# Performance work log

Measured on AMD Instinct MI355X. Metric: run time of the kernel, lower is better.

Reference implementation:

```python
import jax, jax.numpy as jnp
import numpy as np

NUM_LAYER = 5
EMB = 256
N = 100000
E = 300000
SELF_LOOP_BOND = 4
BN_EPS = 1e-5


def setup_inputs() -> dict:
    key = jax.random.key(0)
    ks = jax.random.split(key, 16)
    f = lambda k, shape: jax.random.normal(k, shape, jnp.float32) * 0.02
    return {
        "x_atom": jax.random.randint(ks[0], (N,), 0, 120),
        "x_chir": jax.random.randint(ks[1], (N,), 0, 3),
        "edge_index": jax.random.randint(ks[2], (2, E), 0, N),
        "edge_bond": jax.random.randint(ks[3], (E,), 0, 4),
        "edge_dir": jax.random.randint(ks[4], (E,), 0, 3),
        "atom_emb": f(ks[5], (120, EMB)),
        "chir_emb": f(ks[6], (3, EMB)),
        "bond_embs": f(ks[7], (NUM_LAYER, 6, EMB)),
        "dir_embs": f(ks[8], (NUM_LAYER, 3, EMB)),
        "W1s": f(ks[9], (NUM_LAYER, 2 * EMB, EMB)),
        "b1s": f(ks[10], (NUM_LAYER, 2 * EMB)),
        "W2s": f(ks[11], (NUM_LAYER, EMB, 2 * EMB)),
        "b2s": f(ks[12], (NUM_LAYER, EMB)),
        "bn_w": jnp.ones((NUM_LAYER, EMB), jnp.float32),
        "bn_b": jnp.zeros((NUM_LAYER, EMB), jnp.float32),
    }


def reference(x_atom, x_chir, edge_index, edge_bond, edge_dir,
              atom_emb, chir_emb, bond_embs, dir_embs,
              W1s, b1s, W2s, b2s, bn_w, bn_b):
    n = x_atom.shape[0]
    src, dst = edge_index[0], edge_index[1]
    # add self loops (edge_attr = [4, 0] for each node)
    loop = jnp.arange(n)
    src_full = jnp.concatenate([src, loop])          # [E+N]
    dst_full = jnp.concatenate([dst, loop])          # [E+N]
    bond_full = jnp.concatenate([edge_bond, jnp.full((n,), SELF_LOOP_BOND, edge_bond.dtype)])
    dir_full = jnp.concatenate([edge_dir, jnp.zeros((n,), edge_dir.dtype)])

    # initial node features: atom + chirality embeddings
    h = atom_emb[x_atom] + chir_emb[x_chir]          # [N, EMB]

    for l in range(NUM_LAYER):
        # per-layer edge embeddings (bond type + bond direction)
        e_emb = bond_embs[l][bond_full] + dir_embs[l][dir_full]   # [E+N, EMB]
        # message = x_j + edge_attr; aggregate = scatter-add to dst
        msg = h[src_full] + e_emb                                  # gather
        agg = jax.ops.segment_sum(msg, dst_full, num_segments=n)  # scatter-add
        # update MLP: Linear(EMB->2EMB) -> ReLU -> Linear(2EMB->EMB)
        hmid = jax.nn.relu(agg @ W1s[l].T + b1s[l])                # [N, 2EMB]
        h2 = hmid @ W2s[l].T + b2s[l]                              # [N, EMB]
        # batch norm (training mode: batch statistics, biased variance)
        mean = h2.mean(axis=0)
        var = h2.var(axis=0)
        h2 = (h2 - mean) * jax.lax.rsqrt(var + BN_EPS) * bn_w[l] + bn_b[l]
        # relu on all but last layer; dropout with p=0 is identity
        if l < NUM_LAYER - 1:
            h2 = jax.nn.relu(h2)
        h = h2
    # JK == 'last'
    return h
```

## Files before the change

kernel.cpp:

```cpp
#include <hip/hip_runtime.h>

#define EMB 256
#define NLAYER 5
#define CHUNK 1024

typedef unsigned int u32;
typedef unsigned short u16;

typedef __bf16 bf16x8 __attribute__((ext_vector_type(8)));
typedef float f32x4 __attribute__((ext_vector_type(4)));

__device__ __forceinline__ float bf2f(u16 u) {
    union { u32 i; float f; } x; x.i = ((u32)u) << 16; return x.f;
}
__device__ __forceinline__ u16 f2bf(float f) {
    union { float f; u32 i; } x; x.f = f;
    u32 r = x.i + 0x7FFFu + ((x.i >> 16) & 1u);
    return (u16)(r >> 16);
}
__device__ __forceinline__ void unpack4(uint2 p, float* o) {
    union { u32 i; float f; } a, b, c, d;
    a.i = p.x << 16; b.i = p.x & 0xFFFF0000u;
    c.i = p.y << 16; d.i = p.y & 0xFFFF0000u;
    o[0] = a.f; o[1] = b.f; o[2] = c.f; o[3] = d.f;
}

__global__ void k_detect(const u32* __restrict__ bnw_raw, int* __restrict__ flag) {
    if (threadIdx.x == 0 && blockIdx.x == 0)
        *flag = (bnw_raw[0] == 0x3F803F80u) ? 1 : 0;
}

struct Cvt { const void* s; u16* d; int n; };
struct CvtTab { Cvt t[10]; };

__global__ void k_convert(CvtTab tab, const int* __restrict__ flag, int maxn) {
    int f = *flag;
    int stride = gridDim.x * blockDim.x;
    for (int i = blockIdx.x * blockDim.x + threadIdx.x; i < maxn; i += stride) {
        for (int j = 0; j < 10; j++) {
            if (i < tab.t[j].n) {
                u16 v;
                if (f) v = ((const u16*)tab.t[j].s)[i];
                else   v = f2bf(((const float*)tab.t[j].s)[i]);
                tab.t[j].d[i] = v;
            }
        }
    }
}

__global__ void k_zero(u32* p, int n) {
    int i = blockIdx.x * blockDim.x + threadIdx.x;
    if (i < n) p[i] = 0u;
}

__global__ void k_hist(const int* __restrict__ eidx, const int* __restrict__ ebond,
                       const int* __restrict__ edir,
                       u32* __restrict__ cnt, u32* __restrict__ cntb, u32* __restrict__ cntd, int E) {
    int e = blockIdx.x * blockDim.x + threadIdx.x;
    if (e >= E) return;
    int dst = eidx[E + e];
    atomicAdd(&cnt[dst], 1u);
    atomicAdd(&cntb[dst * 4 + ebond[e]], 1u);
    atomicAdd(&cntd[dst * 3 + edir[e]], 1u);
}

__global__ void k_chunksum(const u32* __restrict__ cnt, u32* __restrict__ partial, int N) {
    int b = blockIdx.x, t = threadIdx.x;
    int base = b * CHUNK + t * 4;
    u32 s = 0;
    for (int i = 0; i < 4; i++) { int idx = base + i; if (idx < N) s += cnt[idx]; }
    __shared__ u32 red[256];
    red[t] = s; __syncthreads();
    for (int o = 128; o > 0; o >>= 1) { if (t < o) red[t] += red[t + o]; __syncthreads(); }
    if (t == 0) partial[b] = red[0];
}

__global__ void k_scanpartial(u32* partial, u32* indptr, int nch, int N) {
    if (threadIdx.x == 0 && blockIdx.x == 0) {
        u32 run = 0;
        for (int i = 0; i < nch; i++) { u32 x = partial[i]; partial[i] = run; run += x; }
        indptr[N] = run;
    }
}

__global__ void k_chunkscan(const u32* __restrict__ cnt, const u32* __restrict__ partial,
                            u32* __restrict__ indptr, u32* __restrict__ fillp, int N) {
    int b = blockIdx.x, t = threadIdx.x;
    int base = b * CHUNK + t * 4;
    u32 c[4]; u32 tsum = 0;
    for (int i = 0; i < 4; i++) { int idx = base + i; c[i] = (idx < N) ? cnt[idx] : 0u; tsum += c[i]; }
    __shared__ u32 sc[256];
    sc[t] = tsum; __syncthreads();
    for (int o = 1; o < 256; o <<= 1) {
        u32 x = (t >= o) ? sc[t - o] : 0u;
        __syncthreads();
        sc[t] += x;
        __syncthreads();
    }
    u32 run = partial[b] + sc[t] - tsum;
    for (int i = 0; i < 4; i++) {
        int idx = base + i;
        if (idx < N) { indptr[idx] = run; fillp[idx] = run; }
        run += c[i];
    }
}

__global__ void k_fill(const int* __restrict__ eidx, u32* __restrict__ fillp,
                       u32* __restrict__ srcs, int E) {
    int e = blockIdx.x * blockDim.x + threadIdx.x;
    if (e >= E) return;
    int dst = eidx[E + e];
    u32 pos = atomicAdd(&fillp[dst], 1u);
    srcs[pos] = (u32)eidx[e];
}

__global__ void k_h0(const int* __restrict__ xa, const int* __restrict__ xc,
                     const u16* __restrict__ aemb, const u16* __restrict__ cemb,
                     u16* __restrict__ H, int N) {
    int wave = threadIdx.x >> 6, lane = threadIdx.x & 63;
    int v = blockIdx.x * 4 + wave;
    if (v >= N) return;
    int a = xa[v], c = xc[v];
    int c4 = lane * 4;
    uint2 pa = *(const uint2*)(aemb + (size_t)a * EMB + c4);
    uint2 pc = *(const uint2*)(cemb + (size_t)c * EMB + c4);
    float fa[4], fc[4];
    unpack4(pa, fa); unpack4(pc, fc);
    ushort4 ov;
    ov.x = f2bf(fa[0] + fc[0]); ov.y = f2bf(fa[1] + fc[1]);
    ov.z = f2bf(fa[2] + fc[2]); ov.w = f2bf(fa[3] + fc[3]);
    *(ushort4*)(H + (size_t)v * EMB + c4) = ov;
}

__global__ void k_scatter(const u16* __restrict__ H, const u32* __restrict__ indptr,
                          const u32* __restrict__ srcs,
                          const u32* __restrict__ cntb, const u32* __restrict__ cntd,
                          const u16* __restrict__ bemb, const u16* __restrict__ demb,
                          const float* __restrict__ scsh, int relu,
                          u16* __restrict__ AGG, int N) {
    int wave = threadIdx.x >> 6, lane = threadIdx.x & 63;
    int v = blockIdx.x * 4 + wave;
    if (v >= N) return;
    int c4 = lane * 4;
    float sc[4] = {1.f, 1.f, 1.f, 1.f}, sh[4] = {0.f, 0.f, 0.f, 0.f};
    if (scsh) {
        float4 s0 = *(const float4*)(scsh + c4);
        float4 s1 = *(const float4*)(scsh + 256 + c4);
        sc[0] = s0.x; sc[1] = s0.y; sc[2] = s0.z; sc[3] = s0.w;
        sh[0] = s1.x; sh[1] = s1.y; sh[2] = s1.z; sh[3] = s1.w;
    }
    float acc[4] = {0.f, 0.f, 0.f, 0.f};
    u32 beg = indptr[v], end = indptr[v + 1];
    for (u32 e = beg; e < end; e++) {
        u32 s = srcs[e];
        uint2 p = *(const uint2*)(H + (size_t)s * EMB + c4);
        float f[4]; unpack4(p, f);
        for (int i = 0; i < 4; i++) {
            float y = f[i] * sc[i] + sh[i];
            if (relu) y = fmaxf(y, 0.f);
            acc[i] += y;
        }
    }
    {
        uint2 p = *(const uint2*)(H + (size_t)v * EMB + c4);
        float f[4]; unpack4(p, f);
        for (int i = 0; i < 4; i++) {
            float y = f[i] * sc[i] + sh[i];
            if (relu) y = fmaxf(y, 0.f);
            acc[i] += y;
        }
    }
    float cb[5];
    cb[0] = (float)cntb[v * 4 + 0]; cb[1] = (float)cntb[v * 4 + 1];
    cb[2] = (float)cntb[v * 4 + 2]; cb[3] = (float)cntb[v * 4 + 3]; cb[4] = 1.f;
    float cd[3];
    cd[0] = (float)cntd[v * 3 + 0] + 1.f; cd[1] = (float)cntd[v * 3 + 1]; cd[2] = (float)cntd[v * 3 + 2];
    for (int b = 0; b < 5; b++) {
        uint2 p = *(const uint2*)(bemb + b * EMB + c4);
        float f[4]; unpack4(p, f);
        for (int i = 0; i < 4; i++) acc[i] += cb[b] * f[i];
    }
    for (int d = 0; d < 3; d++) {
        uint2 p = *(const uint2*)(demb + d * EMB + c4);
        float f[4]; unpack4(p, f);
        for (int i = 0; i < 4; i++) acc[i] += cd[d] * f[i];
    }
    ushort4 ov;
    ov.x = f2bf(acc[0]); ov.y = f2bf(acc[1]); ov.z = f2bf(acc[2]); ov.w = f2bf(acc[3]);
    *(ushort4*)(AGG + (size_t)v * EMB + c4) = ov;
}

#define KP1 264
#define KB1 40

__global__ __launch_bounds__(256) void k_gemm1(
    const u16* __restrict__ A, const u16* __restrict__ W1, const u16* __restrict__ bias,
    u16* __restrict__ HM, int M) {
    __shared__ __align__(16) u16 As[128 * KP1];
    __shared__ __align__(16) u16 Bs[128 * KB1];
    int m0 = blockIdx.x * 128;
    int t = threadIdx.x;
    int wave = t >> 6, lane = t & 63;
    int wm = (wave >> 1) * 64, wn = (wave & 1) * 64;
    int lr = lane & 15, quad = lane >> 4;

    for (int it = 0; it < 16; it++) {
        int ci = t + it * 256;
        int r = ci >> 5, kc = (ci & 31) * 8;
        int gr = m0 + r; if (gr > M - 1) gr = M - 1;
        *(uint4*)(As + r * KP1 + kc) = *(const uint4*)(A + (size_t)gr * 256 + kc);
    }
    __syncthreads();

    for (int nc = 0; nc < 4; nc++) {
        int n0 = nc * 128;
        f32x4 acc[4][4];
        for (int i = 0; i < 4; i++)
            for (int j = 0; j < 4; j++)
                acc[i][j] = (f32x4){0.f, 0.f, 0.f, 0.f};
        for (int ks = 0; ks < 256; ks += 32) {
            __syncthreads();
            for (int it = 0; it < 2; it++) {
                int ci = t + it * 256;
                int r = ci >> 2, kc = (ci & 3) * 8;
                *(uint4*)(Bs + r * KB1 + kc) = *(const uint4*)(W1 + (size_t)(n0 + r) * 256 + ks + kc);
            }
            __syncthreads();
            bf16x8 af[4], bfr[4];
            for (int i = 0; i < 4; i++)
                af[i] = *(const bf16x8*)(As + (wm + i * 16 + lr) * KP1 + ks + quad * 8);
            for (int j = 0; j < 4; j++)
                bfr[j] = *(const bf16x8*)(Bs + (wn + j * 16 + lr) * KB1 + quad * 8);
            for (int i = 0; i < 4; i++)
                for (int j = 0; j < 4; j++)
                    acc[i][j] = __builtin_amdgcn_mfma_f32_16x16x32_bf16(af[i], bfr[j], acc[i][j], 0, 0, 0);
        }
        for (int j = 0; j < 4; j++) {
            int gn = n0 + wn + j * 16 + lr;
            float bv = bf2f(bias[gn]);
            for (int i = 0; i < 4; i++) {
                int mbase = m0 + wm + i * 16 + quad * 4;
                for (int r = 0; r < 4; r++) {
                    int gm = mbase + r;
                    if (gm < M) {
                        float v = fmaxf(acc[i][j][r] + bv, 0.f);
                        HM[(size_t)gm * 512 + gn] = f2bf(v);
                    }
                }
            }
        }
    }
}

#define LSTR 80

__global__ __launch_bounds__(256) void k_gemm2(
    const u16* __restrict__ A, const u16* __restrict__ B, const u16* __restrict__ bias,
    u16* __restrict__ C, float* __restrict__ S, int M) {
    __shared__ __align__(16) u16 As[128 * LSTR];
    __shared__ __align__(16) u16 Bs[128 * LSTR];
    int n0 = blockIdx.x * 128;
    int m0 = blockIdx.y * 128;
    int t = threadIdx.x;
    int wave = t >> 6, lane = t & 63;
    int wm = (wave >> 1) * 64, wn = (wave & 1) * 64;
    int lr = lane & 15, quad = lane >> 4;

    f32x4 acc[4][4];
    for (int i = 0; i < 4; i++)
        for (int j = 0; j < 4; j++)
            acc[i][j] = (f32x4){0.f, 0.f, 0.f, 0.f};

    for (int k0 = 0; k0 < 512; k0 += 64) {
        for (int it = 0; it < 4; it++) {
            int ci = t + it * 256;
            int r = ci >> 3, kc = (ci & 7) * 8;
            int gr = m0 + r; if (gr > M - 1) gr = M - 1;
            *(uint4*)(As + r * LSTR + kc) = *(const uint4*)(A + (size_t)gr * 512 + k0 + kc);
            *(uint4*)(Bs + r * LSTR + kc) = *(const uint4*)(B + (size_t)(n0 + r) * 512 + k0 + kc);
        }
        __syncthreads();
        for (int ks = 0; ks < 64; ks += 32) {
            bf16x8 af[4], bfr[4];
            for (int i = 0; i < 4; i++)
                af[i] = *(const bf16x8*)(As + (wm + i * 16 + lr) * LSTR + ks + quad * 8);
            for (int j = 0; j < 4; j++)
                bfr[j] = *(const bf16x8*)(Bs + (wn + j * 16 + lr) * LSTR + ks + quad * 8);
            for (int i = 0; i < 4; i++)
                for (int j = 0; j < 4; j++)
                    acc[i][j] = __builtin_amdgcn_mfma_f32_16x16x32_bf16(af[i], bfr[j], acc[i][j], 0, 0, 0);
        }
        __syncthreads();
    }
    for (int j = 0; j < 4; j++) {
        int gn = n0 + wn + j * 16 + lr;
        float bv = bf2f(bias[gn]);
        float s = 0.f, q = 0.f;
        for (int i = 0; i < 4; i++) {
            int mbase = m0 + wm + i * 16 + quad * 4;
            for (int r = 0; r < 4; r++) {
                int gm = mbase + r;
                if (gm < M) {
                    float v = acc[i][j][r] + bv;
                    C[(size_t)gm * 256 + gn] = f2bf(v);
                    s += v; q += v * v;
                }
            }
        }
        s += __shfl_xor(s, 16, 64); s += __shfl_xor(s, 32, 64);
        q += __shfl_xor(q, 16, 64); q += __shfl_xor(q, 32, 64);
        if (quad == 0) {
            atomicAdd(&S[gn], s);
            atomicAdd(&S[256 + gn], q);
        }
    }
}

__global__ void k_finalize(const float* __restrict__ S, const u16* __restrict__ bnw,
                           const u16* __restrict__ bnb, float* __restrict__ scsh, float invN) {
    int c = threadIdx.x;
    float mean = S[c] * invN;
    float var = S[256 + c] * invN - mean * mean;
    var = fmaxf(var, 0.f);
    float inv = rsqrtf(var + 1e-5f);
    float sc = bf2f(bnw[c]) * inv;
    scsh[c] = sc;
    scsh[256 + c] = bf2f(bnb[c]) - mean * sc;
}

__global__ void k_out(const u16* __restrict__ H2, const float* __restrict__ scsh,
                      void* __restrict__ out, const int* __restrict__ flag, int N) {
    int wave = threadIdx.x >> 6, lane = threadIdx.x & 63;
    int v = blockIdx.x * 4 + wave;
    if (v >= N) return;
    int c4 = lane * 4;
    float4 s0 = *(const float4*)(scsh + c4);
    float4 s1 = *(const float4*)(scsh + 256 + c4);
    uint2 p = *(const uint2*)(H2 + (size_t)v * EMB + c4);
    float f[4]; unpack4(p, f);
    float o0 = f[0] * s0.x + s1.x;
    float o1 = f[1] * s0.y + s1.y;
    float o2 = f[2] * s0.z + s1.z;
    float o3 = f[3] * s0.w + s1.w;
    if (*flag) {
        ushort4 ov;
        ov.x = f2bf(o0); ov.y = f2bf(o1); ov.z = f2bf(o2); ov.w = f2bf(o3);
        *(ushort4*)((u16*)out + (size_t)v * EMB + c4) = ov;
    } else {
        float4 ov = make_float4(o0, o1, o2, o3);
        *(float4*)((float*)out + (size_t)v * EMB + c4) = ov;
    }
}

extern "C" void kernel_launch(void* const* d_in, const int* in_sizes, int n_in,
                              void* d_out, int out_size, void* d_ws, size_t ws_size,
                              hipStream_t stream) {
    const int* x_atom = (const int*)d_in[0];
    const int* x_chir = (const int*)d_in[1];
    const int* eidx   = (const int*)d_in[2];
    const int* ebond  = (const int*)d_in[3];
    const int* edir   = (const int*)d_in[4];

    const int N = in_sizes[0];
    const int E = in_sizes[3];

    char* p = (char*)d_ws;
    size_t off = 0;
    auto alloc = [&](size_t bytes) -> void* {
        void* r = p + off;
        off += bytes;
        off = (off + 255) & ~(size_t)255;
        return r;
    };
    u16* X   = (u16*)alloc((size_t)N * EMB * 2);
    u16* Y   = (u16*)alloc((size_t)N * EMB * 2);
    u16* HM  = (u16*)alloc((size_t)N * 512 * 2);
    u32* cz  = (u32*)alloc(((size_t)8 * N + NLAYER * 512) * 4);
    u32* cnt  = cz;
    u32* cntb = cz + N;
    u32* cntd = cz + 5 * (size_t)N;
    float* stats5 = (float*)(cz + 8 * (size_t)N);
    u32* indptr = (u32*)alloc((size_t)(N + 1) * 4);
    u32* fillp  = (u32*)alloc((size_t)N * 4);
    u32* srcs   = (u32*)alloc((size_t)E * 4);
    u32* partial = (u32*)alloc(256 * 4);
    float* scsh  = (float*)alloc(512 * 4);
    int* flag    = (int*)alloc(256);

    int csz[10] = {120 * EMB, 3 * EMB, NLAYER * 6 * EMB, NLAYER * 3 * EMB,
                   NLAYER * 512 * EMB, NLAYER * 512, NLAYER * EMB * 512, NLAYER * EMB,
                   NLAYER * EMB, NLAYER * EMB};
    u16* cbuf[10];
    for (int j = 0; j < 10; j++) cbuf[j] = (u16*)alloc((size_t)csz[j] * 2);
    u16* atom_emb  = cbuf[0];
    u16* chir_emb  = cbuf[1];
    u16* bond_embs = cbuf[2];
    u16* dir_embs  = cbuf[3];
    u16* W1s = cbuf[4];
    u16* b1s = cbuf[5];
    u16* W2s = cbuf[6];
    u16* b2s = cbuf[7];
    u16* bnw = cbuf[8];
    u16* bnb = cbuf[9];

    const int nodeBlocks = (N + 3) / 4;
    const int nch = (N + CHUNK - 1) / CHUNK;

    k_detect<<<1, 64, 0, stream>>>((const u32*)d_in[13], flag);
    {
        CvtTab tab;
        int maxn = 0;
        for (int j = 0; j < 10; j++) {
            tab.t[j].s = d_in[5 + j];
            tab.t[j].d = cbuf[j];
            tab.t[j].n = csz[j];
            if (csz[j] > maxn) maxn = csz[j];
        }
        k_convert<<<(maxn + 255) / 256, 256, 0, stream>>>(tab, flag, maxn);
    }

    {
        int z = 8 * N + NLAYER * 512;
        k_zero<<<(z + 255) / 256, 256, 0, stream>>>(cz, z);
    }
    k_hist<<<(E + 255) / 256, 256, 0, stream>>>(eidx, ebond, edir, cnt, cntb, cntd, E);
    k_chunksum<<<nch, 256, 0, stream>>>(cnt, partial, N);
    k_scanpartial<<<1, 64, 0, stream>>>(partial, indptr, nch, N);
    k_chunkscan<<<nch, 256, 0, stream>>>(cnt, partial, indptr, fillp, N);
    k_fill<<<(E + 255) / 256, 256, 0, stream>>>(eidx, fillp, srcs, E);

    k_h0<<<nodeBlocks, 256, 0, stream>>>(x_atom, x_chir, atom_emb, chir_emb, X, N);

    u16* H = X;
    u16* A = Y;
    const int mTiles = (N + 127) / 128;
    for (int l = 0; l < NLAYER; l++) {
        const u16* bemb = bond_embs + (size_t)l * 6 * EMB;
        const u16* demb = dir_embs + (size_t)l * 3 * EMB;
        const u16* W1 = W1s + (size_t)l * 512 * EMB;
        const u16* B1 = b1s + (size_t)l * 512;
        const u16* W2 = W2s + (size_t)l * EMB * 512;
        const u16* B2 = b2s + (size_t)l * EMB;
        float* stats = stats5 + (size_t)l * 512;

        k_scatter<<<nodeBlocks, 256, 0, stream>>>(H, indptr, srcs, cntb, cntd, bemb, demb,
                                                  (l == 0) ? nullptr : scsh, (l == 0) ? 0 : 1,
                                                  A, N);
        k_gemm1<<<mTiles, 256, 0, stream>>>(A, W1, B1, HM, N);
        {
            dim3 g(2, mTiles);
            k_gemm2<<<g, 256, 0, stream>>>(HM, W2, B2, A, stats, N);
        }
        k_finalize<<<1, 256, 0, stream>>>(stats, bnw + (size_t)l * EMB, bnb + (size_t)l * EMB,
                                          scsh, 1.0f / (float)N);
        u16* tmp = H; H = A; A = tmp;
    }

    k_out<<<nodeBlocks, 256, 0, stream>>>(H, scsh, d_out, flag, N);
}
```

Measured before the change: 1.290 ms.

## Fuse the two MLP GEMMs into one kernel with the hidden tile in LDS

Replaces the separate k_gemm1 and k_gemm2 kernels with one k_fused kernel per 64-row tile. It computes the 512-wide ReLU hidden layer in two 256-column halves, stages each half in shared memory, and accumulates the second GEMM straight away. This removes the N×512 bf16 intermediate buffer, its global write and read-back, and one launch per layer. In exchange, weight fragments are read straight from global memory (relying on cache) instead of staged in LDS. Tiles are smaller, with launch bounds set for 2 blocks per CU, which may expose load latency inside the MFMA loop.

Result: slower. 1.316 ms (+2.0%).

```diff
diff --git a/kernel.cpp b/kernel.cpp
--- a/kernel.cpp
+++ b/kernel.cpp
@@ -190,118 +190,105 @@
     *(ushort4*)(AGG + (size_t)v * EMB + c4) = ov;
 }
 
-#define KP1 264
-#define KB1 40
-
-__global__ __launch_bounds__(256) void k_gemm1(
-    const u16* __restrict__ A, const u16* __restrict__ W1, const u16* __restrict__ bias,
-    u16* __restrict__ HM, int M) {
-    __shared__ __align__(16) u16 As[128 * KP1];
-    __shared__ __align__(16) u16 Bs[128 * KB1];
-    int m0 = blockIdx.x * 128;
+#define KP 264
+
+__global__ __launch_bounds__(256, 2) void k_fused(
+    const u16* __restrict__ A, const u16* __restrict__ W1, const u16* __restrict__ b1,
+    const u16* __restrict__ W2, const u16* __restrict__ b2,
+    u16* __restrict__ C, float* __restrict__ S, int M) {
+    __shared__ __align__(16) u16 As[64 * KP];
+    __shared__ __align__(16) u16 Hs[64 * KP];
+    int m0 = blockIdx.x * 64;
     int t = threadIdx.x;
     int wave = t >> 6, lane = t & 63;
-    int wm = (wave >> 1) * 64, wn = (wave & 1) * 64;
+    int wn = wave * 64;
     int lr = lane & 15, quad = lane >> 4;
 
-    for (int it = 0; it < 16; it++) {
+    for (int it = 0; it < 8; it++) {
         int ci = t + it * 256;
         int r = ci >> 5, kc = (ci & 31) * 8;
         int gr = m0 + r; if (gr > M - 1) gr = M - 1;
-        *(uint4*)(As + r * KP1 + kc) = *(const uint4*)(A + (size_t)gr * 256 + kc);
-    }
+        *(uint4*)(As + r * KP + kc) = *(const uint4*)(A + (size_t)gr * 256 + kc);
+    }
+
+    f32x4 acc2[4][4];
+    #pragma unroll
+    for (int i = 0; i < 4; i++)
+        #pragma unroll
+        for (int j = 0; j < 4; j++)
+            acc2[i][j] = (f32x4){0.f, 0.f, 0.f, 0.f};
+
     __syncthreads();
 
-    for (int nc = 0; nc < 4; nc++) {
-        int n0 = nc * 128;
-        f32x4 acc[4][4];
+    #pragma unroll
+    for (int nh = 0; nh < 2; nh++) {
+        f32x4 acc1[4][4];
+        #pragma unroll
         for (int i = 0; i < 4; i++)
+            #pragma unroll
             for (int j = 0; j < 4; j++)
-                acc[i][j] = (f32x4){0.f, 0.f, 0.f, 0.f};
+                acc1[i][j] = (f32x4){0.f, 0.f, 0.f, 0.f};
+        const u16* W1h = W1 + (size_t)(nh * 256) * 256;
+        #pragma unroll
         for (int ks = 0; ks < 256; ks += 32) {
-            __syncthreads();
-            for (int it = 0; it < 2; it++) {
-                int ci = t + it * 256;
-                int r = ci >> 2, kc = (ci & 3) * 8;
-                *(uint4*)(Bs + r * KB1 + kc) = *(const uint4*)(W1 + (size_t)(n0 + r) * 256 + ks + kc);
-            }
-            __syncthreads();
             bf16x8 af[4], bfr[4];
+            #pragma unroll
             for (int i = 0; i < 4; i++)
-                af[i] = *(const bf16x8*)(As + (wm + i * 16 + lr) * KP1 + ks + quad * 8);
+                af[i] = *(const bf16x8*)(As + (i * 16 + lr) * KP + ks + quad * 8);
+            #pragma unroll
             for (int j = 0; j < 4; j++)
-                bfr[j] = *(const bf16x8*)(Bs + (wn + j * 16 + lr) * KB1 + quad * 8);
+                bfr[j] = *(const bf16x8*)(W1h + (size_t)(wn + j * 16 + lr) * 256 + ks + quad * 8);
+            #pragma unroll
             for (int i = 0; i < 4; i++)
+                #pragma unroll
                 for (int j = 0; j < 4; j++)
-                    acc[i][j] = __builtin_amdgcn_mfma_f32_16x16x32_bf16(af[i], bfr[j], acc[i][j], 0, 0, 0);
-        }
+                    acc1[i][j] = __builtin_amdgcn_mfma_f32_16x16x32_bf16(af[i], bfr[j], acc1[i][j], 0, 0, 0);
+        }
+        __syncthreads();
+        #pragma unroll
         for (int j = 0; j < 4; j++) {
-            int gn = n0 + wn + j * 16 + lr;
-            float bv = bf2f(bias[gn]);
-            for (int i = 0; i < 4; i++) {
-                int mbase = m0 + wm + i * 16 + quad * 4;
+            int hn = wn + j * 16 + lr;
+            float bv = bf2f(b1[nh * 256 + hn]);
+            #pragma unroll
+            for (int i = 0; i < 4; i++)
+                #pragma unroll
                 for (int r = 0; r < 4; r++) {
-                    int gm = mbase + r;
-                    if (gm < M) {
-                        float v = fmaxf(acc[i][j][r] + bv, 0.f);
-                        HM[(size_t)gm * 512 + gn] = f2bf(v);
-                    }
+                    float v = fmaxf(acc1[i][j][r] + bv, 0.f);
+                    Hs[(i * 16 + quad * 4 + r) * KP + hn] = f2bf(v);
                 }
-            }
-        }
-    }
-}
-
-#define LSTR 80
-
-__global__ __launch_bounds__(256) void k_gemm2(
-    const u16* __restrict__ A, const u16* __restrict__ B, const u16* __restrict__ bias,
-    u16* __restrict__ C, float* __restrict__ S, int M) {
-    __shared__ __align__(16) u16 As[128 * LSTR];
-    __shared__ __align__(16) u16 Bs[128 * LSTR];
-    int n0 = blockIdx.x * 128;
-    int m0 = blockIdx.y * 128;
-    int t = threadIdx.x;
-    int wave = t >> 6, lane = t & 63;
-    int wm = (wave >> 1) * 64, wn = (wave & 1) * 64;
-    int lr = lane & 15, quad = lane >> 4;
-
-    f32x4 acc[4][4];
-    for (int i = 0; i < 4; i++)
-        for (int j = 0; j < 4; j++)
-            acc[i][j] = (f32x4){0.f, 0.f, 0.f, 0.f};
-
-    for (int k0 = 0; k0 < 512; k0 += 64) {
-        for (int it = 0; it < 4; it++) {
-            int ci = t + it * 256;
-            int r = ci >> 3, kc = (ci & 7) * 8;
-            int gr = m0 + r; if (gr > M - 1) gr = M - 1;
-            *(uint4*)(As + r * LSTR + kc) = *(const uint4*)(A + (size_t)gr * 512 + k0 + kc);
-            *(uint4*)(Bs + r * LSTR + kc) = *(const uint4*)(B + (size_t)(n0 + r) * 512 + k0 + kc);
         }
         __syncthreads();
-        for (int ks = 0; ks < 64; ks += 32) {
+        const u16* W2h = W2 + nh * 256;
+        #pragma unroll
+        for (int ks = 0; ks < 256; ks += 32) {
             bf16x8 af[4], bfr[4];
+            #pragma unroll
             for (int i = 0; i < 4; i++)
-                af[i] = *(const bf16x8*)(As + (wm + i * 16 + lr) * LSTR + ks + quad * 8);
+                af[i] = *(const bf16x8*)(Hs + (i * 16 + lr) * KP + ks + quad * 8);
+            #pragma unroll
             for (int j = 0; j < 4; j++)
-                bfr[j] = *(const bf16x8*)(Bs + (wn + j * 16 + lr) * LSTR + ks + quad * 8);
+                bfr[j] = *(const bf16x8*)(W2h + (size_t)(wn + j * 16 + lr) * 512 + ks + quad * 8);
+            #pragma unroll
             for (int i = 0; i < 4; i++)
+                #pragma unroll
                 for (int j = 0; j < 4; j++)
-                    acc[i][j] = __builtin_amdgcn_mfma_f32_16x16x32_bf16(af[i], bfr[j], acc[i][j], 0, 0, 0);
-        }
-        __syncthreads();
-    }
+                    acc2[i][j] = __builtin_amdgcn_mfma_f32_16x16x32_bf16(af[i], bfr[j], acc2[i][j], 0, 0, 0);
+        }
+    }
+
+    #pragma unroll
     for (int j = 0; j < 4; j++) {
-        int gn = n0 + wn + j * 16 + lr;
-        float bv = bf2f(bias[gn]);
+        int gn = wn + j * 16 + lr;
+        float bv = bf2f(b2[gn]);
         float s = 0.f, q = 0.f;
+        #pragma unroll
         for (int i = 0; i < 4; i++) {
-            int mbase = m0 + wm + i * 16 + quad * 4;
+            int mbase = m0 + i * 16 + quad * 4;
+            #pragma unroll
             for (int r = 0; r < 4; r++) {
                 int gm = mbase + r;
                 if (gm < M) {
-                    float v = acc[i][j][r] + bv;
+                    float v = acc2[i][j][r] + bv;
                     C[(size_t)gm * 256 + gn] = f2bf(v);
                     s += v; q += v * v;
                 }
@@ -374,7 +361,6 @@
     };
     u16* X   = (u16*)alloc((size_t)N * EMB * 2);
     u16* Y   = (u16*)alloc((size_t)N * EMB * 2);
-    u16* HM  = (u16*)alloc((size_t)N * 512 * 2);
     u32* cz  = (u32*)alloc(((size_t)8 * N + NLAYER * 512) * 4);
     u32* cnt  = cz;
     u32* cntb = cz + N;
@@ -433,7 +419,7 @@
 
     u16* H = X;
     u16* A = Y;
-    const int mTiles = (N + 127) / 128;
+    const int mT64 = (N + 63) / 64;
     for (int l = 0; l < NLAYER; l++) {
         const u16* bemb = bond_embs + (size_t)l * 6 * EMB;
         const u16* demb = dir_embs + (size_t)l * 3 * EMB;
@@ -446,11 +432,7 @@
         k_scatter<<<nodeBlocks, 256, 0, stream>>>(H, indptr, srcs, cntb, cntd, bemb, demb,
                                                   (l == 0) ? nullptr : scsh, (l == 0) ? 0 : 1,
                                                   A, N);
-        k_gemm1<<<mTiles, 256, 0, stream>>>(A, W1, B1, HM, N);
-        {
-            dim3 g(2, mTiles);
-            k_gemm2<<<g, 256, 0, stream>>>(HM, W2, B2, A, stats, N);
-        }
+        k_fused<<<mT64, 256, 0, stream>>>(A, W1, B1, W2, B2, A, stats, N);
         k_finalize<<<1, 256, 0, stream>>>(stats, bnw + (size_t)l * EMB, bnb + (size_t)l * EMB,
                                           scsh, 1.0f / (float)N);
         u16* tmp = H; H = A; A = tmp;
```
